# Kernel optimization log

Measured on AMD Instinct MI355X. Metric: run time of the kernel, lower is better.

The kernel has to match this reference:

```python
import jax, jax.numpy as jnp
import numpy as np

RES_SCALE = 1.0

def prelu(x, a):
    return jnp.maximum(x, 0) + a * jnp.minimum(x, 0)

def conv1x1_prelu(x, w, b, a):
    # x: [N,C,H,W], w: [O,C], b: [O]
    y = jnp.einsum('nchw,oc->nohw', x, w) + b[None, :, None, None]
    return prelu(y, a)

def setup_inputs() -> dict:
    key = jax.random.key(0)
    ks = jax.random.split(key, 5)
    N, C, H, W = 2, 128, 96, 96
    Cr = C // 2  # reduction = 2
    return {
        'x':  jax.random.normal(ks[0], (N, C, H, W), jnp.float32),
        'w1': jax.random.normal(ks[1], (Cr, C), jnp.float32) * (1.0 / np.sqrt(C)),
        'b1': jnp.zeros((Cr,), jnp.float32),
        'a1': jnp.asarray(0.25, jnp.float32),
        'w2': jax.random.normal(ks[2], (Cr, C), jnp.float32) * (1.0 / np.sqrt(C)),
        'b2': jnp.zeros((Cr,), jnp.float32),
        'a2': jnp.asarray(0.25, jnp.float32),
        'wa': jax.random.normal(ks[3], (C, C), jnp.float32) * (1.0 / np.sqrt(C)),
        'ba': jnp.zeros((C,), jnp.float32),
        'aa': jnp.asarray(0.25, jnp.float32),
    }

def reference(x, w1, b1, a1, w2, b2, a2, wa, ba, aa):
    N, C, H, W = x.shape
    q = conv1x1_prelu(x, w1, b1, a1)   # [N,Cr,H,W]
    k = conv1x1_prelu(x, w2, b2, a2)   # [N,Cr,H,W]
    v = conv1x1_prelu(x, wa, ba, aa)   # [N,C,H,W]
    Cr = q.shape[1]
    L = H * W
    q = q.transpose(0, 2, 3, 1).reshape(N, L, Cr)   # [N,L,Cr]
    k = k.reshape(N, Cr, L)                          # [N,Cr,L]
    score = jax.nn.softmax(jnp.matmul(q, k), axis=2)  # [N,L,L]
    v = v.reshape(N, C, L).transpose(0, 2, 1)        # [N,L,C]
    out = jnp.matmul(score, v)                        # [N,L,C]
    out = out.transpose(0, 2, 1).reshape(N, C, H, W)
    return out + RES_SCALE * x
```

## Files before the change

### kernel.cpp

```cpp
#include <hip/hip_runtime.h>

#define N_  2
#define C_  128
#define CR_ 64
#define H_  96
#define W_  96
#define L_  (H_*W_)
#define QBLK 128
#define KVBLK 64
#define NQB (L_/QBLK)
#define SPLITS 8
#define TILES_PER ((L_/KVBLK)/SPLITS)
#define NCHUNK (N_*NQB*SPLITS)
#define LOG2E 1.44269504088896f

typedef short bf16x8 __attribute__((ext_vector_type(8)));
typedef float f32x4  __attribute__((ext_vector_type(4)));

static __device__ __forceinline__ float exp2_fast(float x) {
    return __builtin_amdgcn_exp2f(x);
}

static __device__ __forceinline__ unsigned short f2bf(float f) {
    unsigned u = __builtin_bit_cast(unsigned, f);
    unsigned rounding = 0x7FFFu + ((u >> 16) & 1u);
    return (unsigned short)((u + rounding) >> 16);
}

static __device__ __forceinline__ unsigned cvt_pk_bf16(float lo, float hi) {
    unsigned r;
    asm("v_cvt_pk_bf16_f32 %0, %1, %2" : "=v"(r) : "v"(lo), "v"(hi));
    return r;
}

static __device__ __forceinline__ float bf2f(unsigned short s) {
    return __builtin_bit_cast(float, ((unsigned)s) << 16);
}

static __device__ __forceinline__ int sigma_(int r) {
    return (r & 0x23) | ((r & 0x0C) << 1) | ((r & 0x10) >> 2);
}

#define GLD16(G, Ld) __builtin_amdgcn_global_load_lds( \
    (const __attribute__((address_space(1))) void*)(G), \
    (__attribute__((address_space(3))) void*)(Ld), 16, 0, 0)

__global__ __launch_bounds__(256) void wconv_kernel(
    const float* __restrict__ w1, const float* __restrict__ b1, const float* __restrict__ a1,
    const float* __restrict__ w2, const float* __restrict__ b2, const float* __restrict__ a2,
    const float* __restrict__ wa, const float* __restrict__ ba, const float* __restrict__ aa,
    unsigned short* __restrict__ Wbf,
    float* __restrict__ bias, float* __restrict__ alpha, float* __restrict__ scale)
{
    const int idx = blockIdx.x * 256 + threadIdx.x;
    const int o = idx >> 7, k = idx & 127;
    float wv;
    if (o < 64)       wv = w1[o*C_ + k];
    else if (o < 128) wv = w2[(o-64)*C_ + k];
    else              wv = wa[(o-128)*C_ + k];
    Wbf[idx] = f2bf(wv);
    if (blockIdx.x == 0) {
        int t = threadIdx.x;
        float b, a, sc;
        if (t < 64)       { b = b1[t];       a = a1[0]; sc = LOG2E; }
        else if (t < 128) { b = b2[t-64];    a = a2[0]; sc = 1.0f; }
        else              { b = ba[t-128];   a = aa[0]; sc = 1.0f; }
        bias[t] = b; alpha[t] = a; scale[t] = sc;
    }
}

__global__ __launch_bounds__(256) void proj_mfma_kernel(
    const float* __restrict__ x,
    const unsigned short* __restrict__ Wbf,
    const float* __restrict__ bias,
    const float* __restrict__ alpha,
    const float* __restrict__ scale,
    unsigned short* __restrict__ qkv)
{
    __shared__ alignas(16) unsigned char xs[64 * 256];

    const int blk  = blockIdx.x;
    const int n    = blk / (L_/64);
    const int i0   = (blk % (L_/64)) * 64;
    const float* xb = x + (size_t)n * C_ * L_;
    const int tid  = threadIdx.x;
    const int wv_  = tid >> 6;
    const int lane = tid & 63;
    const int lhi  = lane >> 4;
    const int llo  = lane & 15;

    {
        const int i = lane;
        #pragma unroll
        for (int p = 0; p < 8; p++) {
            int c0 = wv_*4 + p*16;
            float v0 = xb[(size_t)(c0+0)*L_ + i0 + i];
            float v1 = xb[(size_t)(c0+1)*L_ + i0 + i];
            float v2 = xb[(size_t)(c0+2)*L_ + i0 + i];
            float v3 = xb[(size_t)(c0+3)*L_ + i0 + i];
            uint2 pk2;
            pk2.x = cvt_pk_bf16(v0, v1);
            pk2.y = cvt_pk_bf16(v2, v3);
            int byte = i*256 + ((((c0 >> 3) ^ (i & 7))) << 4) + (c0 & 7) * 2;
            *reinterpret_cast<uint2*>(xs + byte) = pk2;
        }
    }
    __syncthreads();

    bf16x8 xf[4][4];
    #pragma unroll
    for (int it = 0; it < 4; it++) {
        int i = it*16 + llo;
        #pragma unroll
        for (int ks = 0; ks < 4; ks++) {
            int byte = i*256 + (((ks*4 + lhi) ^ (i & 7)) << 4);
            xf[it][ks] = *reinterpret_cast<const bf16x8*>(xs + byte);
        }
    }

    unsigned short* q_t = qkv;
    unsigned short* k_t = qkv + (size_t)N_ * L_ * CR_;
    unsigned short* v   = qkv + (size_t)2 * N_ * L_ * CR_;
    unsigned short* qtb = q_t + (size_t)n * L_ * CR_;
    unsigned short* ktb = k_t + (size_t)n * L_ * CR_;
    unsigned short* vb  = v   + (size_t)n * C_ * L_;

    #pragma unroll
    for (int oo = 0; oo < 2; oo++) {
        const int ot = wv_*2 + oo;
        const unsigned short* wrow = Wbf + (size_t)(ot*16 + llo) * 128;
        bf16x8 wf[4];
        #pragma unroll
        for (int ks = 0; ks < 4; ks++)
            wf[ks] = *reinterpret_cast<const bf16x8*>(wrow + ks*32 + lhi*8);
        f32x4 acc[4];
        #pragma unroll
        for (int it = 0; it < 4; it++) acc[it] = f32x4{0.f, 0.f, 0.f, 0.f};
        #pragma unroll
        for (int ks = 0; ks < 4; ks++)
            #pragma unroll
            for (int it = 0; it < 4; it++)
                acc[it] = __builtin_amdgcn_mfma_f32_16x16x32_bf16(wf[ks], xf[it][ks], acc[it], 0, 0, 0);

        const int ob = ot*16 + lhi*4;
        const float4 b4 = *reinterpret_cast<const float4*>(bias  + ob);
        const float4 a4 = *reinterpret_cast<const float4*>(alpha + ob);
        const float4 s4 = *reinterpret_cast<const float4*>(scale + ob);
        unsigned short* dst = (ot < 4) ? qtb : ktb;
        const int col = (ot & 3)*16 + lhi*4;
        #pragma unroll
        for (int it = 0; it < 4; it++) {
            int i = i0 + it*16 + llo;
            float y0 = acc[it][0] + b4.x; y0 = (fmaxf(y0,0.f) + a4.x*fminf(y0,0.f))*s4.x;
            float y1 = acc[it][1] + b4.y; y1 = (fmaxf(y1,0.f) + a4.y*fminf(y1,0.f))*s4.y;
            float y2 = acc[it][2] + b4.z; y2 = (fmaxf(y2,0.f) + a4.z*fminf(y2,0.f))*s4.z;
            float y3 = acc[it][3] + b4.w; y3 = (fmaxf(y3,0.f) + a4.w*fminf(y3,0.f))*s4.w;
            uint2 pk2;
            pk2.x = cvt_pk_bf16(y0, y1);
            pk2.y = cvt_pk_bf16(y2, y3);
            *reinterpret_cast<uint2*>(dst + (size_t)i * CR_ + col) = pk2;
        }
    }

    #pragma unroll
    for (int oo = 0; oo < 2; oo++) {
        const int ot2 = wv_*2 + oo;
        const int op  = ot2*16 + llo;
        const unsigned short* wrow = Wbf + (size_t)(128 + op) * 128;
        bf16x8 wf[4];
        #pragma unroll
        for (int ks = 0; ks < 4; ks++)
            wf[ks] = *reinterpret_cast<const bf16x8*>(wrow + ks*32 + lhi*8);
        f32x4 acc[4];
        #pragma unroll
        for (int it = 0; it < 4; it++) acc[it] = f32x4{0.f, 0.f, 0.f, 0.f};
        #pragma unroll
        for (int ks = 0; ks < 4; ks++)
            #pragma unroll
            for (int it = 0; it < 4; it++)
                acc[it] = __builtin_amdgcn_mfma_f32_16x16x32_bf16(xf[it][ks], wf[ks], acc[it], 0, 0, 0);

        const float b = bias[128 + op];
        const float a = alpha[128 + op];
        #pragma unroll
        for (int it = 0; it < 4; it++) {
            float y0 = acc[it][0] + b; y0 = fmaxf(y0,0.f) + a*fminf(y0,0.f);
            float y1 = acc[it][1] + b; y1 = fmaxf(y1,0.f) + a*fminf(y1,0.f);
            float y2 = acc[it][2] + b; y2 = fmaxf(y2,0.f) + a*fminf(y2,0.f);
            float y3 = acc[it][3] + b; y3 = fmaxf(y3,0.f) + a*fminf(y3,0.f);
            uint2 pk2;
            pk2.x = cvt_pk_bf16(y0, y1);
            pk2.y = cvt_pk_bf16(y2, y3);
            *reinterpret_cast<uint2*>(vb + (size_t)op * L_ + i0 + it*16 + lhi*4) = pk2;
        }
    }
}

__global__ __launch_bounds__(256, 3) void attn_kernel(
    const unsigned short* __restrict__ qkv,
    unsigned short* __restrict__ o_part,
    float* __restrict__ l_part)
{
    __shared__ alignas(16) unsigned char kv_lds[2][24*1024];

    const unsigned short* q_t = qkv;
    const unsigned short* k_t = qkv + (size_t)N_ * L_ * CR_;
    const unsigned short* v   = qkv + (size_t)2 * N_ * L_ * CR_;

    const int blk  = blockIdx.x;
    const int n    = blk / (NQB * SPLITS);
    const int rem  = blk % (NQB * SPLITS);
    const int qbi  = rem / SPLITS;
    const int s    = rem % SPLITS;
    const int qb   = qbi * QBLK;
    const int tid  = threadIdx.x;
    const int wave = tid >> 6;
    const int lane = tid & 63;
    const int lhi  = lane >> 4;
    const int llo  = lane & 15;

    const int jb_beg = s * TILES_PER * KVBLK;
    const int jb_end = jb_beg + TILES_PER * KVBLK;

    const unsigned short* qtb = q_t + (size_t)n * L_ * CR_;
    const unsigned short* ktb = k_t + (size_t)n * L_ * CR_;
    const unsigned short* vb  = v   + (size_t)n * C_ * L_;

    bf16x8 qf[2][2];
    #pragma unroll
    for (int st = 0; st < 2; st++) {
        int row = qb + wave * 32 + st * 16 + llo;
        #pragma unroll
        for (int ks = 0; ks < 2; ks++)
            qf[st][ks] = *reinterpret_cast<const bf16x8*>(qtb + (size_t)row * CR_ + ks*32 + lhi*8);
    }

    const int l8 = lane >> 3;
    const int l7 = (lane & 7) * 16;
    const int rho0 = wave*16 + l8;
    const int rho1 = rho0 + 8;
    const unsigned short* kbase0 = ktb + (size_t)sigma_(rho0) * CR_ + ((l7 ^ ((rho0 & 7) << 4)) >> 1);
    const unsigned short* kbase1 = ktb + (size_t)sigma_(rho1) * CR_ + ((l7 ^ ((rho1 & 7) << 4)) >> 1);
    const unsigned short* vbase[4];
    #pragma unroll
    for (int vt = 0; vt < 4; vt++) {
        int c = wave*32 + vt*8 + l8;
        vbase[vt] = vb + (size_t)c * L_ + ((l7 ^ (l8 << 4)) >> 1);
    }

    #define STAGE(b, jb_) do {                                                   \
        GLD16(kbase0 + (size_t)(jb_) * CR_, &kv_lds[b][(wave*2+0)*1024 + 0]);    \
        GLD16(kbase1 + (size_t)(jb_) * CR_, &kv_lds[b][(wave*2+1)*1024 + 0]);    \
        GLD16(vbase[0] + (jb_), &kv_lds[b][8192 + (wave*4+0)*1024]);             \
        GLD16(vbase[1] + (jb_), &kv_lds[b][8192 + (wave*4+1)*1024]);             \
        GLD16(vbase[2] + (jb_), &kv_lds[b][8192 + (wave*4+2)*1024]);             \
        GLD16(vbase[3] + (jb_), &kv_lds[b][8192 + (wave*4+3)*1024]);             \
    } while (0)

    f32x4 o_acc[2][8];
    #pragma unroll
    for (int st = 0; st < 2; st++)
        #pragma unroll
        for (int ct = 0; ct < 8; ct++) o_acc[st][ct] = f32x4{0.f, 0.f, 0.f, 0.f};
    float l_run[2] = {0.f, 0.f};

    int cur = 0;
    STAGE(0, jb_beg);
    __syncthreads();

    for (int jb = jb_beg; jb < jb_end; jb += KVBLK) {
        if (jb + KVBLK < jb_end) STAGE(cur ^ 1, jb + KVBLK);

        const unsigned char* kbuf = &kv_lds[cur][0];
        const unsigned char* vbuf = &kv_lds[cur][8192];

        f32x4 sacc[2][4];
        #pragma unroll
        for (int st = 0; st < 2; st++)
            #pragma unroll
            for (int jt = 0; jt < 4; jt++) sacc[st][jt] = f32x4{0.f, 0.f, 0.f, 0.f};
        __builtin_amdgcn_s_setprio(1);
        #pragma unroll
        for (int ks = 0; ks < 2; ks++) {
            #pragma unroll
            for (int jt = 0; jt < 4; jt++) {
                int rho  = jt*16 + llo;
                int colb = ks*64 + lhi*16;
                bf16x8 kf = *reinterpret_cast<const bf16x8*>(
                    kbuf + rho*128 + (colb ^ ((rho & 7) << 4)));
                sacc[0][jt] = __builtin_amdgcn_mfma_f32_16x16x32_bf16(kf, qf[0][ks], sacc[0][jt], 0, 0, 0);
                sacc[1][jt] = __builtin_amdgcn_mfma_f32_16x16x32_bf16(kf, qf[1][ks], sacc[1][jt], 0, 0, 0);
            }
        }
        __builtin_amdgcn_s_setprio(0);

        unsigned pk[2][8];
        #pragma unroll
        for (int st = 0; st < 2; st++) {
            float rs = 0.f;
            #pragma unroll
            for (int jt = 0; jt < 4; jt++) {
                float pa = exp2_fast(sacc[st][jt][0]);
                float pb = exp2_fast(sacc[st][jt][1]);
                float pc = exp2_fast(sacc[st][jt][2]);
                float pd = exp2_fast(sacc[st][jt][3]);
                rs += (pa + pb) + (pc + pd);
                pk[st][jt*2 + 0] = cvt_pk_bf16(pa, pb);
                pk[st][jt*2 + 1] = cvt_pk_bf16(pc, pd);
            }
            l_run[st] += rs;
        }

        __builtin_amdgcn_s_setprio(1);
        #pragma unroll
        for (int ks = 0; ks < 2; ks++) {
            bf16x8 pf0 = *reinterpret_cast<const bf16x8*>(&pk[0][4*ks]);
            bf16x8 pf1 = *reinterpret_cast<const bf16x8*>(&pk[1][4*ks]);
            #pragma unroll
            for (int ct = 0; ct < 8; ct++) {
                int c = ct*16 + llo;
                int colb = ks*64 + lhi*16;
                bf16x8 vf = *reinterpret_cast<const bf16x8*>(
                    vbuf + c*128 + (colb ^ ((c & 7) << 4)));
                o_acc[0][ct] = __builtin_amdgcn_mfma_f32_16x16x32_bf16(vf, pf0, o_acc[0][ct], 0, 0, 0);
                o_acc[1][ct] = __builtin_amdgcn_mfma_f32_16x16x32_bf16(vf, pf1, o_acc[1][ct], 0, 0, 0);
            }
        }
        __builtin_amdgcn_s_setprio(0);

        __syncthreads();
        cur ^= 1;
    }
    #undef STAGE

    #pragma unroll
    for (int st = 0; st < 2; st++) {
        l_run[st] += __shfl_xor(l_run[st], 16, 64);
        l_run[st] += __shfl_xor(l_run[st], 32, 64);
    }

    unsigned short* ob = o_part + (size_t)blk * (QBLK*C_);
    float* lb = l_part + (size_t)blk * QBLK;
    #pragma unroll
    for (int st = 0; st < 2; st++) {
        int i_loc = wave*32 + st*16 + llo;
        #pragma unroll
        for (int ct = 0; ct < 8; ct++) {
            int c0 = ct*16 + lhi*4;
            uint2 pkd;
            pkd.x = cvt_pk_bf16(o_acc[st][ct][0], o_acc[st][ct][1]);
            pkd.y = cvt_pk_bf16(o_acc[st][ct][2], o_acc[st][ct][3]);
            *reinterpret_cast<uint2*>(ob + (size_t)i_loc * C_ + c0) = pkd;
        }
        if (lhi == 0) {
            lb[i_loc] = l_run[st];
        }
    }
}

__global__ __launch_bounds__(256) void combine_kernel(
    const unsigned short* __restrict__ o_part,
    const float* __restrict__ l_part,
    const float* __restrict__ x,
    float* __restrict__ out)
{
    __shared__ float invl[32];

    const int blk  = blockIdx.x;
    const int part = blk & 3;
    const int qbi  = (blk >> 2) % NQB;
    const int n    = blk / (4 * NQB);
    const int tid  = threadIdx.x;
    const int i0   = part * 32;

    const size_t pbase = (size_t)(n*NQB + qbi) * SPLITS;

    if (tid < 32) {
        float lt = 0.f;
        for (int s = 0; s < SPLITS; s++)
            lt += l_part[(pbase + s) * QBLK + i0 + tid];
        invl[tid] = 1.0f / lt;
    }
    __syncthreads();

    const int il = tid >> 3;
    const int cg = tid & 7;

    float acc[16];
    #pragma unroll
    for (int k = 0; k < 16; k++) acc[k] = 0.f;

    for (int s = 0; s < SPLITS; s++) {
        const unsigned short* src = o_part + (pbase + s) * (QBLK*C_) + (size_t)(i0 + il) * C_ + cg*16;
        bf16x8 v0 = *reinterpret_cast<const bf16x8*>(src);
        bf16x8 v1 = *reinterpret_cast<const bf16x8*>(src + 8);
        #pragma unroll
        for (int k = 0; k < 8; k++) acc[k]     += bf2f((unsigned short)v0[k]);
        #pragma unroll
        for (int k = 0; k < 8; k++) acc[8 + k] += bf2f((unsigned short)v1[k]);
    }

    const float nv = invl[il];
    const int ig = qbi*QBLK + i0 + il;
    const float* xb = x   + (size_t)n * C_ * L_;
    float*       ob = out + (size_t)n * C_ * L_;
    #pragma unroll
    for (int k = 0; k < 16; k++) {
        int c = cg*16 + k;
        ob[(size_t)c * L_ + ig] = acc[k] * nv + xb[(size_t)c * L_ + ig];
    }
}

extern "C" void kernel_launch(void* const* d_in, const int* in_sizes, int n_in,
                              void* d_out, int out_size, void* d_ws, size_t ws_size,
                              hipStream_t stream) {
    const float* x  = (const float*)d_in[0];
    const float* w1 = (const float*)d_in[1];
    const float* b1 = (const float*)d_in[2];
    const float* a1 = (const float*)d_in[3];
    const float* w2 = (const float*)d_in[4];
    const float* b2 = (const float*)d_in[5];
    const float* a2 = (const float*)d_in[6];
    const float* wa = (const float*)d_in[7];
    const float* ba = (const float*)d_in[8];
    const float* aa = (const float*)d_in[9];
    float* out = (float*)d_out;

    unsigned short* qkv = (unsigned short*)d_ws;
    size_t qkv_bytes = ((size_t)2*N_*L_*CR_ + (size_t)N_*C_*L_) * 2;
    size_t off = (qkv_bytes + 255) & ~(size_t)255;

    unsigned short* o_part = (unsigned short*)((char*)d_ws + off);
    size_t o_elems = (size_t)NCHUNK * QBLK * C_;
    float* l_part = (float*)(o_part + o_elems);
    float* tail   = l_part + (size_t)NCHUNK * QBLK;
    unsigned short* Wbf = (unsigned short*)tail;
    float* bias  = (float*)(Wbf + 256*128);
    float* alpha = bias + 256;
    float* scale = alpha + 256;

    wconv_kernel<<<128, 256, 0, stream>>>(w1, b1, a1, w2, b2, a2, wa, ba, aa,
                                          Wbf, bias, alpha, scale);
    proj_mfma_kernel<<<N_ * (L_/64), 256, 0, stream>>>(x, Wbf, bias, alpha, scale, qkv);
    attn_kernel<<<NCHUNK, 256, 0, stream>>>(qkv, o_part, l_part);
    combine_kernel<<<N_ * NQB * 4, 256, 0, stream>>>(o_part, l_part, x, out);
}
```

Measured before the change: 103.5 us.

## Fuse split-combine into attention via last-block atomic counter; row-sum via MFMA

Removes the separate combine kernel. Each attention block bumps a per-query-tile atomic counter, and the last of the SPLITS blocks reduces the partial outputs, normalizes, adds the residual and writes the output. Softmax row sums are now built with an MFMA against a ones vector on the bf16 probabilities, which replaces the scalar adds and cross-lane shuffles. This saves a kernel launch and its tail, but the combine work now lands serially on the last block of each tile, and the row sum now uses bf16-rounded probabilities.

```diff
diff --git a/kernel.cpp b/kernel.cpp
--- a/kernel.cpp
+++ b/kernel.cpp
@@ -50,7 +50,8 @@
     const float* __restrict__ w2, const float* __restrict__ b2, const float* __restrict__ a2,
     const float* __restrict__ wa, const float* __restrict__ ba, const float* __restrict__ aa,
     unsigned short* __restrict__ Wbf,
-    float* __restrict__ bias, float* __restrict__ alpha, float* __restrict__ scale)
+    float* __restrict__ bias, float* __restrict__ alpha, float* __restrict__ scale,
+    unsigned* __restrict__ tile_done)
 {
     const int idx = blockIdx.x * 256 + threadIdx.x;
     const int o = idx >> 7, k = idx & 127;
@@ -66,6 +67,7 @@
         else if (t < 128) { b = b2[t-64];    a = a2[0]; sc = 1.0f; }
         else              { b = ba[t-128];   a = aa[0]; sc = 1.0f; }
         bias[t] = b; alpha[t] = a; scale[t] = sc;
+        if (t < N_*NQB) tile_done[t] = 0u;
     }
 }
 
@@ -199,9 +201,14 @@
 __global__ __launch_bounds__(256, 3) void attn_kernel(
     const unsigned short* __restrict__ qkv,
     unsigned short* __restrict__ o_part,
-    float* __restrict__ l_part)
+    float* __restrict__ l_part,
+    unsigned* __restrict__ tile_done,
+    const float* __restrict__ x,
+    float* __restrict__ out)
 {
     __shared__ alignas(16) unsigned char kv_lds[2][24*1024];
+    __shared__ unsigned done_s;
+    __shared__ float invl_s[QBLK];
 
     const unsigned short* q_t = qkv;
     const unsigned short* k_t = qkv + (size_t)N_ * L_ * CR_;
@@ -212,6 +219,7 @@
     const int rem  = blk % (NQB * SPLITS);
     const int qbi  = rem / SPLITS;
     const int s    = rem % SPLITS;
+    const int qn   = n * NQB + qbi;
     const int qb   = qbi * QBLK;
     const int tid  = threadIdx.x;
     const int wave = tid >> 6;
@@ -234,6 +242,10 @@
         for (int ks = 0; ks < 2; ks++)
             qf[st][ks] = *reinterpret_cast<const bf16x8*>(qtb + (size_t)row * CR_ + ks*32 + lhi*8);
     }
+
+    bf16x8 ones_f;
+    #pragma unroll
+    for (int e = 0; e < 8; e++) ones_f[e] = (short)0x3F80;
 
     const int l8 = lane >> 3;
     const int l7 = (lane & 7) * 16;
@@ -262,7 +274,9 @@
     for (int st = 0; st < 2; st++)
         #pragma unroll
         for (int ct = 0; ct < 8; ct++) o_acc[st][ct] = f32x4{0.f, 0.f, 0.f, 0.f};
-    float l_run[2] = {0.f, 0.f};
+    f32x4 acc_l[2];
+    acc_l[0] = f32x4{0.f, 0.f, 0.f, 0.f};
+    acc_l[1] = f32x4{0.f, 0.f, 0.f, 0.f};
 
     int cur = 0;
     STAGE(0, jb_beg);
@@ -294,28 +308,30 @@
         }
         __builtin_amdgcn_s_setprio(0);
 
-        unsigned pk[2][8];
-        #pragma unroll
-        for (int st = 0; st < 2; st++) {
-            float rs = 0.f;
-            #pragma unroll
-            for (int jt = 0; jt < 4; jt++) {
-                float pa = exp2_fast(sacc[st][jt][0]);
-                float pb = exp2_fast(sacc[st][jt][1]);
-                float pc = exp2_fast(sacc[st][jt][2]);
-                float pd = exp2_fast(sacc[st][jt][3]);
-                rs += (pa + pb) + (pc + pd);
-                pk[st][jt*2 + 0] = cvt_pk_bf16(pa, pb);
-                pk[st][jt*2 + 1] = cvt_pk_bf16(pc, pd);
-            }
-            l_run[st] += rs;
-        }
+        #pragma unroll
+        for (int st = 0; st < 2; st++)
+            #pragma unroll
+            for (int jt = 0; jt < 4; jt++)
+                #pragma unroll
+                for (int r = 0; r < 4; r++)
+                    sacc[st][jt][r] = exp2_fast(sacc[st][jt][r]);
 
         __builtin_amdgcn_s_setprio(1);
         #pragma unroll
         for (int ks = 0; ks < 2; ks++) {
-            bf16x8 pf0 = *reinterpret_cast<const bf16x8*>(&pk[0][4*ks]);
-            bf16x8 pf1 = *reinterpret_cast<const bf16x8*>(&pk[1][4*ks]);
+            unsigned pw0[4], pw1[4];
+            pw0[0] = cvt_pk_bf16(sacc[0][2*ks][0],   sacc[0][2*ks][1]);
+            pw0[1] = cvt_pk_bf16(sacc[0][2*ks][2],   sacc[0][2*ks][3]);
+            pw0[2] = cvt_pk_bf16(sacc[0][2*ks+1][0], sacc[0][2*ks+1][1]);
+            pw0[3] = cvt_pk_bf16(sacc[0][2*ks+1][2], sacc[0][2*ks+1][3]);
+            pw1[0] = cvt_pk_bf16(sacc[1][2*ks][0],   sacc[1][2*ks][1]);
+            pw1[1] = cvt_pk_bf16(sacc[1][2*ks][2],   sacc[1][2*ks][3]);
+            pw1[2] = cvt_pk_bf16(sacc[1][2*ks+1][0], sacc[1][2*ks+1][1]);
+            pw1[3] = cvt_pk_bf16(sacc[1][2*ks+1][2], sacc[1][2*ks+1][3]);
+            bf16x8 pf0 = *reinterpret_cast<const bf16x8*>(&pw0[0]);
+            bf16x8 pf1 = *reinterpret_cast<const bf16x8*>(&pw1[0]);
+            acc_l[0] = __builtin_amdgcn_mfma_f32_16x16x32_bf16(ones_f, pf0, acc_l[0], 0, 0, 0);
+            acc_l[1] = __builtin_amdgcn_mfma_f32_16x16x32_bf16(ones_f, pf1, acc_l[1], 0, 0, 0);
             #pragma unroll
             for (int ct = 0; ct < 8; ct++) {
                 int c = ct*16 + llo;
@@ -333,12 +349,6 @@
     }
     #undef STAGE
 
-    #pragma unroll
-    for (int st = 0; st < 2; st++) {
-        l_run[st] += __shfl_xor(l_run[st], 16, 64);
-        l_run[st] += __shfl_xor(l_run[st], 32, 64);
-    }
-
     unsigned short* ob = o_part + (size_t)blk * (QBLK*C_);
     float* lb = l_part + (size_t)blk * QBLK;
     #pragma unroll
@@ -352,62 +362,50 @@
             pkd.y = cvt_pk_bf16(o_acc[st][ct][2], o_acc[st][ct][3]);
             *reinterpret_cast<uint2*>(ob + (size_t)i_loc * C_ + c0) = pkd;
         }
-        if (lhi == 0) {
-            lb[i_loc] = l_run[st];
-        }
-    }
-}
-
-__global__ __launch_bounds__(256) void combine_kernel(
-    const unsigned short* __restrict__ o_part,
-    const float* __restrict__ l_part,
-    const float* __restrict__ x,
-    float* __restrict__ out)
-{
-    __shared__ float invl[32];
-
-    const int blk  = blockIdx.x;
-    const int part = blk & 3;
-    const int qbi  = (blk >> 2) % NQB;
-    const int n    = blk / (4 * NQB);
-    const int tid  = threadIdx.x;
-    const int i0   = part * 32;
-
-    const size_t pbase = (size_t)(n*NQB + qbi) * SPLITS;
-
-    if (tid < 32) {
-        float lt = 0.f;
-        for (int s = 0; s < SPLITS; s++)
-            lt += l_part[(pbase + s) * QBLK + i0 + tid];
-        invl[tid] = 1.0f / lt;
-    }
+        if (lhi == 0) lb[i_loc] = acc_l[st][0];
+    }
+
+    __threadfence();
+    if (tid == 0) done_s = atomicAdd(&tile_done[qn], 1u);
     __syncthreads();
-
-    const int il = tid >> 3;
-    const int cg = tid & 7;
-
-    float acc[16];
-    #pragma unroll
-    for (int k = 0; k < 16; k++) acc[k] = 0.f;
-
-    for (int s = 0; s < SPLITS; s++) {
-        const unsigned short* src = o_part + (pbase + s) * (QBLK*C_) + (size_t)(i0 + il) * C_ + cg*16;
-        bf16x8 v0 = *reinterpret_cast<const bf16x8*>(src);
-        bf16x8 v1 = *reinterpret_cast<const bf16x8*>(src + 8);
-        #pragma unroll
-        for (int k = 0; k < 8; k++) acc[k]     += bf2f((unsigned short)v0[k]);
-        #pragma unroll
-        for (int k = 0; k < 8; k++) acc[8 + k] += bf2f((unsigned short)v1[k]);
-    }
-
-    const float nv = invl[il];
-    const int ig = qbi*QBLK + i0 + il;
-    const float* xb = x   + (size_t)n * C_ * L_;
-    float*       ob = out + (size_t)n * C_ * L_;
-    #pragma unroll
-    for (int k = 0; k < 16; k++) {
-        int c = cg*16 + k;
-        ob[(size_t)c * L_ + ig] = acc[k] * nv + xb[(size_t)c * L_ + ig];
+    if (done_s == SPLITS - 1) {
+        __threadfence();
+        const size_t pbase = (size_t)qn * SPLITS;
+        if (tid < QBLK) {
+            float lt = 0.f;
+            for (int sp = 0; sp < SPLITS; sp++)
+                lt += l_part[(pbase + sp) * QBLK + tid];
+            invl_s[tid] = 1.0f / lt;
+        }
+        __syncthreads();
+        const int il = tid & 31;
+        const int cg = tid >> 5;
+        const float* xb2 = x   + (size_t)n * C_ * L_;
+        float*       ob2 = out + (size_t)n * C_ * L_;
+        #pragma unroll
+        for (int part = 0; part < 4; part++) {
+            const int ii = part*32 + il;
+            float acc[16];
+            #pragma unroll
+            for (int k2 = 0; k2 < 16; k2++) acc[k2] = 0.f;
+            for (int sp = 0; sp < SPLITS; sp++) {
+                const unsigned short* src = o_part + (pbase + sp) * (QBLK*C_)
+                                          + (size_t)ii * C_ + cg*16;
+                bf16x8 v0 = *reinterpret_cast<const bf16x8*>(src);
+                bf16x8 v1 = *reinterpret_cast<const bf16x8*>(src + 8);
+                #pragma unroll
+                for (int k2 = 0; k2 < 8; k2++) acc[k2]     += bf2f((unsigned short)v0[k2]);
+                #pragma unroll
+                for (int k2 = 0; k2 < 8; k2++) acc[8 + k2] += bf2f((unsigned short)v1[k2]);
+            }
+            const float nv = invl_s[ii];
+            const int ig = qb + ii;
+            #pragma unroll
+            for (int k2 = 0; k2 < 16; k2++) {
+                int c = cg*16 + k2;
+                ob2[(size_t)c * L_ + ig] = acc[k2] * nv + xb2[(size_t)c * L_ + ig];
+            }
+        }
     }
 }
 
@@ -438,10 +436,10 @@
     float* bias  = (float*)(Wbf + 256*128);
     float* alpha = bias + 256;
     float* scale = alpha + 256;
+    unsigned* tile_done = (unsigned*)(scale + 256);
 
     wconv_kernel<<<128, 256, 0, stream>>>(w1, b1, a1, w2, b2, a2, wa, ba, aa,
-                                          Wbf, bias, alpha, scale);
+                                          Wbf, bias, alpha, scale, tile_done);
     proj_mfma_kernel<<<N_ * (L_/64), 256, 0, stream>>>(x, Wbf, bias, alpha, scale, qkv);
-    attn_kernel<<<NCHUNK, 256, 0, stream>>>(qkv, o_part, l_part);
-    combine_kernel<<<N_ * NQB * 4, 256, 0, stream>>>(o_part, l_part, x, out);
-}
+    attn_kernel<<<NCHUNK, 256, 0, stream>>>(qkv, o_part, l_part, tile_done, x, out);
+}
```

Result: slower. 363.1 us (+250.9%).
